# Kernel tuning notes

Hardware: AMD Instinct MI355X
Metric: run time of the kernel (lower is better)

Reference implementation:

```python
import jax, jax.numpy as jnp
import numpy as np

N, D_IN, D_EMB, K = 16384, 1024, 256, 1024
ALPHA, EPS = 0.01, 1e-5


def setup_inputs() -> dict:
    key = jax.random.key(0)
    ks = jax.random.split(key, 6)
    inp = jax.random.normal(ks[0], (N, D_IN), dtype=jnp.float32)
    W_send = jax.random.normal(ks[1], (D_IN, D_EMB), dtype=jnp.float32) / np.sqrt(D_IN)
    b_send = jnp.zeros((D_EMB,), dtype=jnp.float32)
    W_recv = jax.random.normal(ks[2], (D_EMB, D_IN), dtype=jnp.float32) / np.sqrt(D_EMB)
    b_recv = jnp.zeros((D_IN,), dtype=jnp.float32)
    codebook = jax.random.normal(ks[3], (K, D_EMB), dtype=jnp.float32)
    ema_vecs = codebook.copy()
    ema_size = jnp.zeros((K,), dtype=jnp.float32)
    return {"input": inp, "W_send": W_send, "b_send": b_send,
            "W_recv": W_recv, "b_recv": b_recv, "codebook": codebook,
            "ema_vecs": ema_vecs, "ema_size": ema_size}


def reference(input, W_send, b_send, W_recv, b_recv, codebook, ema_vecs, ema_size):
    sg = jax.lax.stop_gradient
    # send projection -> latent z  [N, D_EMB]
    z = input @ W_send + b_send
    # nearest-neighbor lookup: argmin_k ||e_k||^2 - 2 <z, e_k>
    sqr = jnp.sum(codebook * codebook, axis=1)          # [K]
    cov = jnp.einsum('nj,kj->nk', z, codebook)          # [N, K]
    codes = jnp.argmin(sqr - 2.0 * cov, axis=-1)        # [N] int
    # fetch embeddings (gather)
    vectors = codebook[codes]                            # [N, D_EMB]
    # mse losses, reduction='sum'
    embedding = jnp.sum((vectors - sg(z)) ** 2)
    commitment = jnp.sum((z - sg(vectors)) ** 2)
    # straight-through output
    emb_out = z + sg(vectors - z)
    # EMA accumulate (one-hot scatter == segment_sum)
    upd_vecs = jax.ops.segment_sum(z, codes, num_segments=K)              # [K, D_EMB]
    upd_size = jax.ops.segment_sum(jnp.ones((z.shape[0],), z.dtype), codes, num_segments=K)
    ema_vecs_new = ema_vecs + ALPHA * (upd_vecs - ema_vecs)
    ema_size_new = ema_size + ALPHA * (upd_size - ema_size)
    # EMA update (Laplace-smoothed centroid)
    n = jnp.sum(ema_size_new)
    coef = n / (n + K * EPS)
    size = coef * (ema_size_new + EPS)
    weight_new = ema_vecs_new / size[:, None]
    # empirical entropy of the codes in bits
    prob = jnp.bincount(codes, length=K).astype(jnp.float32) / codes.size
    ent = -jnp.sum(jnp.where(prob > 0, prob * jnp.log(prob), 0.0)) / jnp.log(2.0)
    # recv projection
    x = emb_out @ W_recv + b_recv
    return (x, codes, embedding, commitment, ent, ema_vecs_new, ema_size_new, weight_new)
```

## Files before the change

### kernel.cpp

```cpp
#include <hip/hip_runtime.h>
#include <math.h>

#define NROWS 16384
#define DIN   1024
#define DEMB  256
#define KC    1024
#define ALPHA 0.01f
#define EPSV  1e-5f
#define INV2048 4.8828125e-4f
#define CHUNK 32
#define COV_CHUNKS 8

typedef _Float16 f16;
typedef __attribute__((ext_vector_type(4)))  _Float16 f16x4;
typedef __attribute__((ext_vector_type(8)))  _Float16 f16x8;
typedef __attribute__((ext_vector_type(16))) float    f32x16;
typedef unsigned long long u64;

#define OFF_Z       0
#define OFF_R       4194304
#define OFF_SQR     5242880
#define OFF_ZH      5243904
#define OFF_ZL      7341056
#define OFF_WTH     9438208
#define OFF_WTL     9569280
#define OFF_CBH     9700352
#define OFF_CBL     9831424
#define OFF_KEYS    9962496
#define OFF_CODES   9995264
#define OFF_LIST    10011648
#define OFF_OFFS    10028032
#define OFF_UPD     10029056
#define OFF_HIST    10291200
#define OFF_CURSOR  10292224
#define OFF_LOSS    10293248
#define ZERO_LEN    264208
#define OFF_COUNTSF 10293264
#define OFF_SIZE    10294288

#define OUT_X      0
#define OUT_CODES  16777216
#define OUT_EMB    16793600
#define OUT_COMMIT 16793601
#define OUT_ENT    16793602
#define OUT_EMAV   16793603
#define OUT_EMAS   17055747
#define OUT_W      17056771

__device__ __forceinline__ void split_f32(float x, f16& h, f16& l) {
    h = (f16)x;
    l = (f16)((x - (float)h) * 2048.0f);
}

__global__ __launch_bounds__(64) void sqr_kernel(const float* __restrict__ cb,
                                                 float* __restrict__ sqr) {
    int k = blockIdx.x;
    int lane = threadIdx.x;
    float4 v = ((const float4*)cb)[k * 64 + lane];
    float s = v.x * v.x + v.y * v.y + v.z * v.z + v.w * v.w;
    for (int off = 32; off > 0; off >>= 1) s += __shfl_down(s, off, 64);
    if (lane == 0) sqr[k] = s;
}

__global__ __launch_bounds__(256) void split_wt_kernel(const float* __restrict__ W,
                                                       f16* __restrict__ wth,
                                                       f16* __restrict__ wtl) {
    int n = blockIdx.x;
    int t = threadIdx.x;
    f16x4 h4, l4;
#pragma unroll
    for (int j = 0; j < 4; ++j) {
        int k = t * 4 + j;
        float x = W[(size_t)k * DEMB + n];
        f16 h, l; split_f32(x, h, l);
        h4[j] = h; l4[j] = l;
    }
    *(f16x4*)&wth[(size_t)n * DIN + t * 4] = h4;
    *(f16x4*)&wtl[(size_t)n * DIN + t * 4] = l4;
}

__global__ __launch_bounds__(256) void split_cb_kernel(const float* __restrict__ cb,
                                                       f16* __restrict__ cbh,
                                                       f16* __restrict__ cbl) {
    int idx = (blockIdx.x * 256 + threadIdx.x) * 4;
    float4 v = *(const float4*)&cb[idx];
    f16x4 h4, l4;
    f16 h, l;
    split_f32(v.x, h, l); h4[0] = h; l4[0] = l;
    split_f32(v.y, h, l); h4[1] = h; l4[1] = l;
    split_f32(v.z, h, l); h4[2] = h; l4[2] = l;
    split_f32(v.w, h, l); h4[3] = h; l4[3] = l;
    *(f16x4*)&cbh[idx] = h4;
    *(f16x4*)&cbl[idx] = l4;
}

__global__ __launch_bounds__(512) void gemm1_mfma(const float* __restrict__ in,
                                                  const f16* __restrict__ wth,
                                                  const f16* __restrict__ wtl,
                                                  const float* __restrict__ bsend,
                                                  float* __restrict__ z,
                                                  f16* __restrict__ zh,
                                                  f16* __restrict__ zl) {
    __shared__ f16 sm[2 * 2 * 2 * 128 * 64];
    const int tid = threadIdx.x;
    const int wave = tid >> 6, lane = tid & 63;
    const int half = lane >> 5, l31 = lane & 31;
    const int wrow = wave >> 2, wcol = wave & 3;
    const int rowBase = blockIdx.y * 128;
    const int colBase = blockIdx.x * 128;

    const int sr  = tid >> 2;
    const int skq = tid & 3;
    const int sr7 = sr & 7;

    f32x16 accm[2] = {};
    f32x16 accx[2] = {};

    auto stageB = [&](int buf, int ks) {
#pragma unroll
        for (int i = 0; i < 4; ++i) {
            const int q  = wave * 4 + i;
            const int hl = q >> 4;
            const int c  = (q & 15) * 8 + (lane >> 3);
            const int p  = lane & 7;
            const int s  = p ^ (c & 7);
            const f16* src = (hl ? wtl : wth)
                           + (size_t)(colBase + c) * DIN + ks + s * 8;
            f16* dst = sm + buf * 32768 + 16384 + q * 512 + lane * 8;
            __builtin_amdgcn_global_load_lds(
                (const __attribute__((address_space(1))) void*)src,
                (__attribute__((address_space(3))) void*)dst, 16, 0, 0);
        }
    };

    auto loadA = [&](int ks, float4* av) {
        const float* src = &in[(size_t)(rowBase + sr) * DIN + ks + skq * 16];
#pragma unroll
        for (int j = 0; j < 4; ++j) av[j] = ((const float4*)src)[j];
    };

    auto writeA = [&](int buf, const float4* av) {
        f16* Abase = sm + buf * 32768;
#pragma unroll
        for (int q = 0; q < 2; ++q) {
            f16x8 h8, l8;
#pragma unroll
            for (int j = 0; j < 2; ++j) {
                float4 v = av[q * 2 + j];
                f16 h, l;
                split_f32(v.x, h, l); h8[j * 4 + 0] = h; l8[j * 4 + 0] = l;
                split_f32(v.y, h, l); h8[j * 4 + 1] = h; l8[j * 4 + 1] = l;
                split_f32(v.z, h, l); h8[j * 4 + 2] = h; l8[j * 4 + 2] = l;
                split_f32(v.w, h, l); h8[j * 4 + 3] = h; l8[j * 4 + 3] = l;
            }
            const int s = skq * 2 + q;
            const int off = sr * 64 + ((s ^ sr7) << 3);
            *(f16x8*)&Abase[off] = h8;
            *(f16x8*)&Abase[8192 + off] = l8;
        }
    };

    auto compute = [&](int buf) {
        const f16* Ah = sm + buf * 32768;
        const f16* Al = Ah + 8192;
        const f16* Bh = Ah + 16384;
        const f16* Bl = Ah + 24576;
        const int c  = wcol * 32 + l31;
        const int c7 = c & 7;
#pragma unroll
        for (int t4 = 0; t4 < 4; ++t4) {
            const int s = t4 * 2 + half;
            f16x8 a_h[2], a_l[2];
#pragma unroll
            for (int rt = 0; rt < 2; ++rt) {
                const int r = wrow * 64 + rt * 32 + l31;
                const int off = r * 64 + ((s ^ (r & 7)) << 3);
                a_h[rt] = *(const f16x8*)&Ah[off];
                a_l[rt] = *(const f16x8*)&Al[off];
            }
            const int boff = c * 64 + ((s ^ c7) << 3);
            f16x8 b_h = *(const f16x8*)&Bh[boff];
            f16x8 b_l = *(const f16x8*)&Bl[boff];
#pragma unroll
            for (int rt = 0; rt < 2; ++rt) {
                accm[rt] = __builtin_amdgcn_mfma_f32_32x32x16_f16(a_h[rt], b_h, accm[rt], 0, 0, 0);
                accx[rt] = __builtin_amdgcn_mfma_f32_32x32x16_f16(a_h[rt], b_l, accx[rt], 0, 0, 0);
                accx[rt] = __builtin_amdgcn_mfma_f32_32x32x16_f16(a_l[rt], b_h, accx[rt], 0, 0, 0);
            }
        }
    };

    stageB(0, 0);
    {
        float4 av[4];
        loadA(0, av);
        writeA(0, av);
    }
    __syncthreads();

    int cur = 0;
    for (int step = 0; step < 16; ++step) {
        float4 av[4];
        const bool pf = (step + 1) < 16;
        if (pf) {
            stageB(cur ^ 1, (step + 1) * 64);
            loadA((step + 1) * 64, av);
        }
        compute(cur);
        if (pf) writeA(cur ^ 1, av);
        __syncthreads();
        cur ^= 1;
    }

#pragma unroll
    for (int rt = 0; rt < 2; ++rt) {
        const int col = colBase + wcol * 32 + l31;
        const float bb = bsend[col];
#pragma unroll
        for (int reg = 0; reg < 16; ++reg) {
            const int row = rowBase + wrow * 64 + rt * 32 + (reg & 3) + 8 * (reg >> 2) + 4 * half;
            const float zv = accm[rt][reg] + INV2048 * accx[rt][reg] + bb;
            const size_t o = (size_t)row * DEMB + col;
            z[o] = zv;
            f16 h = (f16)zv;
            zh[o] = h;
            zl[o] = (f16)((zv - (float)h) * 2048.0f);
        }
    }
}

__device__ __forceinline__ void cov_stage(const f16* __restrict__ cbh,
                                          const f16* __restrict__ cbl,
                                          f16* sC, int buf, int codeBase,
                                          int wave, int lane) {
#pragma unroll
    for (int i = 0; i < 8; ++i) {
        const int seg = wave * 8 + i;
        const int hl  = seg >> 4;
        const int rp  = seg & 15;
        const int r   = rp * 2 + (lane >> 5);
        const f16* src = (hl ? cbl : cbh)
                       + (size_t)(codeBase + r) * DEMB
                       + (((lane & 31) ^ r) << 3);
        f16* dst = sC + (((buf << 1) + hl) * 32 + rp * 2) * DEMB;
        __builtin_amdgcn_global_load_lds(
            (const __attribute__((address_space(1))) void*)src,
            (__attribute__((address_space(3))) void*)dst,
            16, 0, 0);
    }
}

__global__ __launch_bounds__(256, 2) void cov_mfma_kernel(const f16* __restrict__ zh,
                                                          const f16* __restrict__ zl,
                                                          const f16* __restrict__ cbh,
                                                          const f16* __restrict__ cbl,
                                                          const float* __restrict__ sqr,
                                                          u64* __restrict__ keys) {
    __shared__ f16 sC[2 * 2 * 32 * DEMB];
    const int tid = threadIdx.x;
    const int wave = tid >> 6, lane = tid & 63;
    const int half = lane >> 5, l31 = lane & 31;
    const int rowBase = blockIdx.y * 128 + wave * 32;
    const int myRow = rowBase + l31;
    const int cb0 = blockIdx.x * (COV_CHUNKS * 32);

    cov_stage(cbh, cbl, sC, 0, cb0, wave, lane);

    f16x8 a_h[16], a_l[16];
#pragma unroll
    for (int t = 0; t < 16; ++t) {
        size_t o = (size_t)myRow * DEMB + t * 16 + half * 8;
        a_h[t] = *(const f16x8*)&zh[o];
        a_l[t] = *(const f16x8*)&zl[o];
    }

    float runv[16];
    int   runc[16];
#pragma unroll
    for (int r = 0; r < 16; ++r) { runv[r] = 3.4e38f; runc[r] = 0; }

    for (int cc = 0; cc < COV_CHUNKS; ++cc) {
        __syncthreads();
        if (cc + 1 < COV_CHUNKS)
            cov_stage(cbh, cbl, sC, (cc + 1) & 1, cb0 + (cc + 1) * 32, wave, lane);

        const f16* Ch = sC + ((cc & 1) * 2 + 0) * 32 * DEMB;
        const f16* Cl = sC + ((cc & 1) * 2 + 1) * 32 * DEMB;

        f32x16 accm = {};
        f32x16 accx = {};
#pragma unroll
        for (int t = 0; t < 16; ++t) {
            const int seg = t * 2 + half;
            const int p = ((seg ^ l31) << 3);
            f16x8 b_h = *(const f16x8*)&Ch[l31 * DEMB + p];
            f16x8 b_l = *(const f16x8*)&Cl[l31 * DEMB + p];
            accm = __builtin_amdgcn_mfma_f32_32x32x16_f16(a_h[t], b_h, accm, 0, 0, 0);
            accx = __builtin_amdgcn_mfma_f32_32x32x16_f16(a_h[t], b_l, accx, 0, 0, 0);
            accx = __builtin_amdgcn_mfma_f32_32x32x16_f16(a_l[t], b_h, accx, 0, 0, 0);
        }

        const int code = cb0 + cc * 32 + l31;
        const float sqv = sqr[code];
#pragma unroll
        for (int r = 0; r < 16; ++r) {
            float s = sqv - 2.0f * (accm[r] + INV2048 * accx[r]);
            if (s < runv[r]) { runv[r] = s; runc[r] = code; }
        }
    }

#pragma unroll
    for (int r = 0; r < 16; ++r) {
        float v = runv[r]; int ci = runc[r];
        for (int off = 16; off > 0; off >>= 1) {
            float ov = __shfl_down(v, off, 32);
            int   oc = __shfl_down(ci, off, 32);
            if (ov < v || (ov == v && oc < ci)) { v = ov; ci = oc; }
        }
        if (l31 == 0) {
            int row = rowBase + (r & 3) + 8 * (r >> 2) + 4 * half;
            unsigned ub = __float_as_uint(v);
            ub = (ub & 0x80000000u) ? ~ub : (ub | 0x80000000u);
            u64 key = ((u64)ub << 32) | (unsigned)ci;
            atomicMin(&keys[row], key);
        }
    }
}

__global__ __launch_bounds__(256) void decode_kernel(const u64* __restrict__ keys,
                                                     int* __restrict__ codes,
                                                     float* __restrict__ out_codes,
                                                     int* __restrict__ hist) {
    int r = blockIdx.x * 256 + threadIdx.x;
    int c = (int)(keys[r] & 0xFFFFFFFFull);
    codes[r] = c;
    out_codes[r] = (float)c;
    atomicAdd(&hist[c], 1);
}

__global__ __launch_bounds__(1024) void prefix_kernel(const int* __restrict__ hist,
                                                      int* __restrict__ offs,
                                                      float* __restrict__ countsf) {
    __shared__ int s[1024];
    int t = threadIdx.x;
    int v = hist[t];
    s[t] = v;
    countsf[t] = (float)v;
    __syncthreads();
    for (int d = 1; d < 1024; d <<= 1) {
        int x = (t >= d) ? s[t - d] : 0;
        __syncthreads();
        s[t] += x;
        __syncthreads();
    }
    offs[t] = s[t] - v;
}

__global__ __launch_bounds__(256) void fill_kernel(const int* __restrict__ codes,
                                                   const int* __restrict__ offs,
                                                   int* __restrict__ cursor,
                                                   int* __restrict__ list) {
    int r = blockIdx.x * 256 + threadIdx.x;
    int c = codes[r];
    int pos = offs[c] + atomicAdd(&cursor[c], 1);
    list[pos] = r;
}

__global__ __launch_bounds__(256) void upd_loss_kernel(const float* __restrict__ z,
                                                       const float* __restrict__ cb,
                                                       const int* __restrict__ list,
                                                       const int* __restrict__ codes,
                                                       float* __restrict__ upd,
                                                       float* __restrict__ loss) {
    __shared__ int srow[CHUNK];
    __shared__ int scode[CHUNK];
    const int tid = threadIdx.x;
    const int base = blockIdx.x * CHUNK;
    if (tid < CHUNK) {
        int r = list[base + tid];
        srow[tid] = r;
        scode[tid] = codes[r];
    }
    __syncthreads();

    int cur = scode[0];
    float cbv = cb[(size_t)cur * DEMB + tid];
    float acc = 0.f, lacc = 0.f;
    float zv = z[(size_t)srow[0] * DEMB + tid];
#pragma unroll 4
    for (int i = 0; i < CHUNK; ++i) {
        float znext = (i + 1 < CHUNK) ? z[(size_t)srow[i + 1] * DEMB + tid] : 0.f;
        int c = scode[i];
        if (c != cur) {
            atomicAdd(&upd[(size_t)cur * DEMB + tid], acc);
            acc = 0.f;
            cur = c;
            cbv = cb[(size_t)cur * DEMB + tid];
        }
        acc += zv;
        float d = zv - cbv;
        lacc += d * d;
        zv = znext;
    }
    atomicAdd(&upd[(size_t)cur * DEMB + tid], acc);

    __shared__ float red[256];
    red[tid] = lacc;
    __syncthreads();
    for (int s = 128; s > 0; s >>= 1) {
        if (tid < s) red[tid] += red[tid + s];
        __syncthreads();
    }
    if (tid == 0) atomicAdd(loss, red[0]);
}

__global__ __launch_bounds__(256) void gemm64_kernel(const float* __restrict__ A,
                                                     const float* __restrict__ B,
                                                     float* __restrict__ C,
                                                     int M, int Kd, int Nc) {
    __shared__ float As[16][68];
    __shared__ float Bs[16][64];
    const int tid = threadIdx.x;
    const int tx = tid & 15, ty = tid >> 4;
    const int rowBase = blockIdx.y * 64;
    const int colBase = blockIdx.x * 64;

    float acc[4][4];
#pragma unroll
    for (int i = 0; i < 4; ++i)
#pragma unroll
        for (int j = 0; j < 4; ++j) acc[i][j] = 0.f;

    const int a_row = tid >> 2;
    const int a_c4  = (tid & 3) * 4;
    const int b_r   = tid >> 4;
    const int b_c4  = (tid & 15) * 4;

    for (int kk = 0; kk < Kd; kk += 16) {
        float4 av = *(const float4*)&A[(size_t)(rowBase + a_row) * Kd + kk + a_c4];
        float4 bv = *(const float4*)&B[(size_t)(kk + b_r) * Nc + colBase + b_c4];
        __syncthreads();
        As[a_c4 + 0][a_row] = av.x;  As[a_c4 + 1][a_row] = av.y;
        As[a_c4 + 2][a_row] = av.z;  As[a_c4 + 3][a_row] = av.w;
        *(float4*)&Bs[b_r][b_c4] = bv;
        __syncthreads();
#pragma unroll
        for (int d = 0; d < 16; ++d) {
            float4 a01 = *(const float4*)&As[d][ty * 4];
            float4 b01 = *(const float4*)&Bs[d][tx * 4];
            float a[4] = {a01.x, a01.y, a01.z, a01.w};
            float b[4] = {b01.x, b01.y, b01.z, b01.w};
#pragma unroll
            for (int i = 0; i < 4; ++i)
#pragma unroll
                for (int j = 0; j < 4; ++j) acc[i][j] += a[i] * b[j];
        }
    }

#pragma unroll
    for (int i = 0; i < 4; ++i) {
        int r = rowBase + ty * 4 + i;
        *(float4*)&C[(size_t)r * Nc + colBase + tx * 4] =
            make_float4(acc[i][0], acc[i][1], acc[i][2], acc[i][3]);
    }
}

__global__ __launch_bounds__(256) void recv_kernel(const float* __restrict__ R,
                                                   const float* __restrict__ brecv,
                                                   const int* __restrict__ codes,
                                                   float* __restrict__ out) {
    const int n = blockIdx.x;
    const int t = threadIdx.x;
    const int code = codes[n];
    float4 r = ((const float4*)(R + (size_t)code * DIN))[t];
    float4 b = ((const float4*)brecv)[t];
    ((float4*)(out + (size_t)n * DIN))[t] =
        make_float4(r.x + b.x, r.y + b.y, r.z + b.z, r.w + b.w);
}

__global__ __launch_bounds__(1024) void ema_small_kernel(const float* __restrict__ ema_size,
                                                         const float* __restrict__ counts,
                                                         const float* __restrict__ loss,
                                                         float* __restrict__ size_ws,
                                                         float* __restrict__ out) {
    __shared__ float rn[1024];
    __shared__ float re[1024];
    const int k = threadIdx.x;
    float c  = counts[k];
    float es = ema_size[k];
    float esn = es + ALPHA * (c - es);
    out[OUT_EMAS + k] = esn;
    float p = c * (1.0f / (float)NROWS);
    rn[k] = esn;
    re[k] = (p > 0.f) ? p * logf(p) : 0.f;
    __syncthreads();
    for (int s = 512; s > 0; s >>= 1) {
        if (k < s) { rn[k] += rn[k + s]; re[k] += re[k + s]; }
        __syncthreads();
    }
    float n = rn[0];
    float coef = n / (n + (float)KC * EPSV);
    size_ws[k] = coef * (esn + EPSV);
    if (k == 0) {
        out[OUT_ENT] = -re[0] / logf(2.0f);
        float l = loss[0];
        out[OUT_EMB] = l;
        out[OUT_COMMIT] = l;
    }
}

__global__ __launch_bounds__(256) void emav_kernel(const float* __restrict__ ema_vecs,
                                                   const float* __restrict__ upd,
                                                   const float* __restrict__ size_ws,
                                                   float* __restrict__ out) {
    int idx = blockIdx.x * 256 + threadIdx.x;
    float ev = ema_vecs[idx], uv = upd[idx];
    float evn = ev + ALPHA * (uv - ev);
    out[OUT_EMAV + idx] = evn;
    out[OUT_W + idx] = evn / size_ws[idx >> 8];
}

extern "C" void kernel_launch(void* const* d_in, const int* in_sizes, int n_in,
                              void* d_out, int out_size, void* d_ws, size_t ws_size,
                              hipStream_t stream) {
    const float* input    = (const float*)d_in[0];
    const float* W_send   = (const float*)d_in[1];
    const float* b_send   = (const float*)d_in[2];
    const float* W_recv   = (const float*)d_in[3];
    const float* b_recv   = (const float*)d_in[4];
    const float* codebook = (const float*)d_in[5];
    const float* ema_vecs = (const float*)d_in[6];
    const float* ema_size = (const float*)d_in[7];
    float* out = (float*)d_out;
    float* ws  = (float*)d_ws;
    int*   wsi = (int*)d_ws;

    f16* wth = (f16*)(ws + OFF_WTH);
    f16* wtl = (f16*)(ws + OFF_WTL);
    f16* cbh = (f16*)(ws + OFF_CBH);
    f16* cbl = (f16*)(ws + OFF_CBL);
    f16* zh  = (f16*)(ws + OFF_ZH);
    f16* zl  = (f16*)(ws + OFF_ZL);
    u64* keys = (u64*)(ws + OFF_KEYS);

    (void)hipMemsetAsync(ws + OFF_UPD, 0, (size_t)ZERO_LEN * sizeof(float), stream);
    (void)hipMemsetAsync(ws + OFF_KEYS, 0xFF, (size_t)NROWS * sizeof(u64), stream);

    sqr_kernel<<<KC, 64, 0, stream>>>(codebook, ws + OFF_SQR);
    split_wt_kernel<<<DEMB, 256, 0, stream>>>(W_send, wth, wtl);
    split_cb_kernel<<<256, 256, 0, stream>>>(codebook, cbh, cbl);

    gemm64_kernel<<<dim3(DIN / 64, KC / 64), 256, 0, stream>>>(
        codebook, W_recv, ws + OFF_R, KC, DEMB, DIN);

    gemm1_mfma<<<dim3(DEMB / 128, NROWS / 128), 512, 0, stream>>>(
        input, wth, wtl, b_send, ws + OFF_Z, zh, zl);

    cov_mfma_kernel<<<dim3(KC / (COV_CHUNKS * 32), NROWS / 128), 256, 0, stream>>>(
        zh, zl, cbh, cbl, ws + OFF_SQR, keys);

    decode_kernel<<<NROWS / 256, 256, 0, stream>>>(
        keys, wsi + OFF_CODES, out + OUT_CODES, wsi + OFF_HIST);

    prefix_kernel<<<1, 1024, 0, stream>>>(
        wsi + OFF_HIST, wsi + OFF_OFFS, ws + OFF_COUNTSF);

    fill_kernel<<<NROWS / 256, 256, 0, stream>>>(
        wsi + OFF_CODES, wsi + OFF_OFFS, wsi + OFF_CURSOR, wsi + OFF_LIST);

    upd_loss_kernel<<<NROWS / CHUNK, 256, 0, stream>>>(
        ws + OFF_Z, codebook, wsi + OFF_LIST, wsi + OFF_CODES,
        ws + OFF_UPD, ws + OFF_LOSS);

    recv_kernel<<<NROWS, 256, 0, stream>>>(
        ws + OFF_R, b_recv, wsi + OFF_CODES, out + OUT_X);

    ema_small_kernel<<<1, 1024, 0, stream>>>(
        ema_size, ws + OFF_COUNTSF, ws + OFF_LOSS, ws + OFF_SIZE, out);

    emav_kernel<<<KC, 256, 0, stream>>>(
        ema_vecs, ws + OFF_UPD, ws + OFF_SIZE, out);
}
```

Before: 277.3 us.

## Fuse prep kernels and memsets, use MFMA for codebook·W_recv, remap block order

Replaces two memsets and three small prep kernels with a single prep_kernel that also splits W_recv into fp16 hi/lo parts and initializes the workspace buffers. The scalar fp32 gemm64 for codebook@W_recv becomes a split-fp16 MFMA kernel (gemm2_mfma) that stages W_recv hi/lo in the zh region before gemm1 overwrites it. gemm1 and cov kernels switch to 1D grids with a swizzled block-to-tile mapping meant to improve L2 reuse. The aim is to cut launch overhead and the cost of the small GEMM, at the price of split-fp16 precision in R.

```diff
diff --git a/kernel.cpp b/kernel.cpp
--- a/kernel.cpp
+++ b/kernel.cpp
@@ -34,7 +34,6 @@
 #define OFF_HIST    10291200
 #define OFF_CURSOR  10292224
 #define OFF_LOSS    10293248
-#define ZERO_LEN    264208
 #define OFF_COUNTSF 10293264
 #define OFF_SIZE    10294288
 
@@ -52,46 +51,78 @@
     l = (f16)((x - (float)h) * 2048.0f);
 }
 
-__global__ __launch_bounds__(64) void sqr_kernel(const float* __restrict__ cb,
-                                                 float* __restrict__ sqr) {
-    int k = blockIdx.x;
-    int lane = threadIdx.x;
-    float4 v = ((const float4*)cb)[k * 64 + lane];
-    float s = v.x * v.x + v.y * v.y + v.z * v.z + v.w * v.w;
-    for (int off = 32; off > 0; off >>= 1) s += __shfl_down(s, off, 64);
-    if (lane == 0) sqr[k] = s;
-}
-
-__global__ __launch_bounds__(256) void split_wt_kernel(const float* __restrict__ W,
-                                                       f16* __restrict__ wth,
-                                                       f16* __restrict__ wtl) {
-    int n = blockIdx.x;
-    int t = threadIdx.x;
-    f16x4 h4, l4;
-#pragma unroll
-    for (int j = 0; j < 4; ++j) {
-        int k = t * 4 + j;
-        float x = W[(size_t)k * DEMB + n];
-        f16 h, l; split_f32(x, h, l);
-        h4[j] = h; l4[j] = l;
-    }
-    *(f16x4*)&wth[(size_t)n * DIN + t * 4] = h4;
-    *(f16x4*)&wtl[(size_t)n * DIN + t * 4] = l4;
-}
-
-__global__ __launch_bounds__(256) void split_cb_kernel(const float* __restrict__ cb,
-                                                       f16* __restrict__ cbh,
-                                                       f16* __restrict__ cbl) {
-    int idx = (blockIdx.x * 256 + threadIdx.x) * 4;
-    float4 v = *(const float4*)&cb[idx];
-    f16x4 h4, l4;
-    f16 h, l;
-    split_f32(v.x, h, l); h4[0] = h; l4[0] = l;
-    split_f32(v.y, h, l); h4[1] = h; l4[1] = l;
-    split_f32(v.z, h, l); h4[2] = h; l4[2] = l;
-    split_f32(v.w, h, l); h4[3] = h; l4[3] = l;
-    *(f16x4*)&cbh[idx] = h4;
-    *(f16x4*)&cbl[idx] = l4;
+__global__ __launch_bounds__(256) void prep_kernel(const float* __restrict__ W_send,
+                                                   const float* __restrict__ W_recv,
+                                                   const float* __restrict__ cb,
+                                                   float* __restrict__ ws) {
+    const int b = blockIdx.x;
+    const int t = threadIdx.x;
+    int* wsi = (int*)ws;
+
+    if (b < 256) {
+        f16* wth = (f16*)(ws + OFF_WTH);
+        f16* wtl = (f16*)(ws + OFF_WTL);
+        const int n = b;
+        f16x4 h4, l4;
+#pragma unroll
+        for (int j = 0; j < 4; ++j) {
+            int k = t * 4 + j;
+            float x = W_send[(size_t)k * DEMB + n];
+            f16 h, l; split_f32(x, h, l);
+            h4[j] = h; l4[j] = l;
+        }
+        *(f16x4*)&wth[(size_t)n * DIN + t * 4] = h4;
+        *(f16x4*)&wtl[(size_t)n * DIN + t * 4] = l4;
+    } else if (b < 512) {
+        f16* cbh = (f16*)(ws + OFF_CBH);
+        f16* cbl = (f16*)(ws + OFF_CBL);
+        int idx = ((b - 256) * 256 + t) * 4;
+        float4 v = *(const float4*)&cb[idx];
+        f16x4 h4, l4;
+        f16 h, l;
+        split_f32(v.x, h, l); h4[0] = h; l4[0] = l;
+        split_f32(v.y, h, l); h4[1] = h; l4[1] = l;
+        split_f32(v.z, h, l); h4[2] = h; l4[2] = l;
+        split_f32(v.w, h, l); h4[3] = h; l4[3] = l;
+        *(f16x4*)&cbh[idx] = h4;
+        *(f16x4*)&cbl[idx] = l4;
+    } else if (b < 768) {
+        f16* wrh = (f16*)(ws + OFF_ZH);
+        f16* wrl = (f16*)(ws + OFF_ZH + 131072);
+        const int n = (b - 512) * 4 + (t >> 6);
+        const int lane = t & 63;
+        f16x4 h4, l4;
+#pragma unroll
+        for (int j = 0; j < 4; ++j) {
+            int k = lane * 4 + j;
+            float x = W_recv[(size_t)k * DIN + n];
+            f16 h, l; split_f32(x, h, l);
+            h4[j] = h; l4[j] = l;
+        }
+        *(f16x4*)&wrh[(size_t)n * DEMB + lane * 4] = h4;
+        *(f16x4*)&wrl[(size_t)n * DEMB + lane * 4] = l4;
+    } else if (b < 1024) {
+        float* sqr = ws + OFF_SQR;
+        const int k = (b - 768) * 4 + (t >> 6);
+        const int lane = t & 63;
+        float4 v = ((const float4*)cb)[k * 64 + lane];
+        float s = v.x * v.x + v.y * v.y + v.z * v.z + v.w * v.w;
+        for (int off = 32; off > 0; off >>= 1) s += __shfl_down(s, off, 64);
+        if (lane == 0) sqr[k] = s;
+    } else if (b < 1280) {
+        float4 zed = make_float4(0.f, 0.f, 0.f, 0.f);
+        *(float4*)&ws[OFF_UPD + (size_t)(b - 1024) * 1024 + t * 4] = zed;
+    } else if (b == 1280) {
+#pragma unroll
+        for (int j = 0; j < 4; ++j) {
+            wsi[OFF_HIST + t * 4 + j] = 0;
+            wsi[OFF_CURSOR + t * 4 + j] = 0;
+        }
+        if (t < 16) ws[OFF_LOSS + t] = 0.f;
+    } else {
+        u64* keys = (u64*)(ws + OFF_KEYS);
+        keys[(b - 1281) * 256 + t] = ~0ull;
+    }
 }
 
 __global__ __launch_bounds__(512) void gemm1_mfma(const float* __restrict__ in,
@@ -106,8 +137,13 @@
     const int wave = tid >> 6, lane = tid & 63;
     const int half = lane >> 5, l31 = lane & 31;
     const int wrow = wave >> 2, wcol = wave & 3;
-    const int rowBase = blockIdx.y * 128;
-    const int colBase = blockIdx.x * 128;
+
+    const int L = blockIdx.x;
+    const int v = L >> 3;
+    const int bx = v & 1;
+    const int by = (L & 7) + 8 * (v >> 1);
+    const int rowBase = by * 128;
+    const int colBase = bx * 128;
 
     const int sr  = tid >> 2;
     const int skq = tid & 3;
@@ -146,12 +182,12 @@
             f16x8 h8, l8;
 #pragma unroll
             for (int j = 0; j < 2; ++j) {
-                float4 v = av[q * 2 + j];
+                float4 v4 = av[q * 2 + j];
                 f16 h, l;
-                split_f32(v.x, h, l); h8[j * 4 + 0] = h; l8[j * 4 + 0] = l;
-                split_f32(v.y, h, l); h8[j * 4 + 1] = h; l8[j * 4 + 1] = l;
-                split_f32(v.z, h, l); h8[j * 4 + 2] = h; l8[j * 4 + 2] = l;
-                split_f32(v.w, h, l); h8[j * 4 + 3] = h; l8[j * 4 + 3] = l;
+                split_f32(v4.x, h, l); h8[j * 4 + 0] = h; l8[j * 4 + 0] = l;
+                split_f32(v4.y, h, l); h8[j * 4 + 1] = h; l8[j * 4 + 1] = l;
+                split_f32(v4.z, h, l); h8[j * 4 + 2] = h; l8[j * 4 + 2] = l;
+                split_f32(v4.w, h, l); h8[j * 4 + 3] = h; l8[j * 4 + 3] = l;
             }
             const int s = skq * 2 + q;
             const int off = sr * 64 + ((s ^ sr7) << 3);
@@ -226,6 +262,67 @@
             zh[o] = h;
             zl[o] = (f16)((zv - (float)h) * 2048.0f);
         }
+    }
+}
+
+__global__ __launch_bounds__(256, 2) void gemm2_mfma(const f16* __restrict__ cbh,
+                                                     const f16* __restrict__ cbl,
+                                                     const f16* __restrict__ wrh,
+                                                     const f16* __restrict__ wrl,
+                                                     float* __restrict__ R) {
+    __shared__ f16 sm[16384];
+    const int tid = threadIdx.x;
+    const int wave = tid >> 6, lane = tid & 63;
+    const int half = lane >> 5, l31 = lane & 31;
+    const int wr = wave >> 1, wc = wave & 1;
+    const int rowBase = blockIdx.y * 64;
+    const int colBase = blockIdx.x * 64;
+
+    f32x16 accm = {}, accx = {};
+
+    for (int step = 0; step < 4; ++step) {
+        const int ks = step * 64;
+        __syncthreads();
+#pragma unroll
+        for (int i = 0; i < 8; ++i) {
+            const int q   = wave * 8 + i;
+            const int arr = q >> 3;
+            const int grp = q & 7;
+            const int r   = grp * 8 + (lane >> 3);
+            const int p   = lane & 7;
+            const int s   = p ^ (r & 7);
+            const f16* basep = (arr == 0) ? cbh : (arr == 1) ? cbl
+                             : (arr == 2) ? wrh : wrl;
+            const int rowg = ((arr >= 2) ? colBase : rowBase) + r;
+            const f16* src = basep + (size_t)rowg * DEMB + ks + s * 8;
+            f16* dst = sm + arr * 4096 + grp * 512;
+            __builtin_amdgcn_global_load_lds(
+                (const __attribute__((address_space(1))) void*)src,
+                (__attribute__((address_space(3))) void*)dst, 16, 0, 0);
+        }
+        __syncthreads();
+#pragma unroll
+        for (int t = 0; t < 4; ++t) {
+            const int sgi = t * 2 + half;
+            const int ar = wr * 32 + l31;
+            const int bc = wc * 32 + l31;
+            const int aoff = ar * 64 + ((sgi ^ (ar & 7)) << 3);
+            const int boff = bc * 64 + ((sgi ^ (bc & 7)) << 3);
+            f16x8 a_h = *(const f16x8*)&sm[aoff];
+            f16x8 a_l = *(const f16x8*)&sm[4096 + aoff];
+            f16x8 b_h = *(const f16x8*)&sm[8192 + boff];
+            f16x8 b_l = *(const f16x8*)&sm[12288 + boff];
+            accm = __builtin_amdgcn_mfma_f32_32x32x16_f16(a_h, b_h, accm, 0, 0, 0);
+            accx = __builtin_amdgcn_mfma_f32_32x32x16_f16(a_h, b_l, accx, 0, 0, 0);
+            accx = __builtin_amdgcn_mfma_f32_32x32x16_f16(a_l, b_h, accx, 0, 0, 0);
+        }
+    }
+
+    const int col = colBase + wc * 32 + l31;
+#pragma unroll
+    for (int reg = 0; reg < 16; ++reg) {
+        const int row = rowBase + wr * 32 + (reg & 3) + 8 * (reg >> 2) + 4 * half;
+        R[(size_t)row * DIN + col] = accm[reg] + INV2048 * accx[reg];
     }
 }
 
@@ -260,9 +357,15 @@
     const int tid = threadIdx.x;
     const int wave = tid >> 6, lane = tid & 63;
     const int half = lane >> 5, l31 = lane & 31;
-    const int rowBase = blockIdx.y * 128 + wave * 32;
+
+    const int L = blockIdx.x;
+    const int v = L >> 3;
+    const int bx = v & 3;
+    const int by = (L & 7) + 8 * (v >> 2);
+
+    const int rowBase = by * 128 + wave * 32;
     const int myRow = rowBase + l31;
-    const int cb0 = blockIdx.x * (COV_CHUNKS * 32);
+    const int cb0 = bx * (COV_CHUNKS * 32);
 
     cov_stage(cbh, cbl, sC, 0, cb0, wave, lane);
 
@@ -311,15 +414,15 @@
 
 #pragma unroll
     for (int r = 0; r < 16; ++r) {
-        float v = runv[r]; int ci = runc[r];
+        float v2 = runv[r]; int ci = runc[r];
         for (int off = 16; off > 0; off >>= 1) {
-            float ov = __shfl_down(v, off, 32);
+            float ov = __shfl_down(v2, off, 32);
             int   oc = __shfl_down(ci, off, 32);
-            if (ov < v || (ov == v && oc < ci)) { v = ov; ci = oc; }
+            if (ov < v2 || (ov == v2 && oc < ci)) { v2 = ov; ci = oc; }
         }
         if (l31 == 0) {
             int row = rowBase + (r & 3) + 8 * (r >> 2) + 4 * half;
-            unsigned ub = __float_as_uint(v);
+            unsigned ub = __float_as_uint(v2);
             ub = (ub & 0x80000000u) ? ~ub : (ub | 0x80000000u);
             u64 key = ((u64)ub << 32) | (unsigned)ci;
             atomicMin(&keys[row], key);
@@ -412,57 +515,6 @@
         __syncthreads();
     }
     if (tid == 0) atomicAdd(loss, red[0]);
-}
-
-__global__ __launch_bounds__(256) void gemm64_kernel(const float* __restrict__ A,
-                                                     const float* __restrict__ B,
-                                                     float* __restrict__ C,
-                                                     int M, int Kd, int Nc) {
-    __shared__ float As[16][68];
-    __shared__ float Bs[16][64];
-    const int tid = threadIdx.x;
-    const int tx = tid & 15, ty = tid >> 4;
-    const int rowBase = blockIdx.y * 64;
-    const int colBase = blockIdx.x * 64;
-
-    float acc[4][4];
-#pragma unroll
-    for (int i = 0; i < 4; ++i)
-#pragma unroll
-        for (int j = 0; j < 4; ++j) acc[i][j] = 0.f;
-
-    const int a_row = tid >> 2;
-    const int a_c4  = (tid & 3) * 4;
-    const int b_r   = tid >> 4;
-    const int b_c4  = (tid & 15) * 4;
-
-    for (int kk = 0; kk < Kd; kk += 16) {
-        float4 av = *(const float4*)&A[(size_t)(rowBase + a_row) * Kd + kk + a_c4];
-        float4 bv = *(const float4*)&B[(size_t)(kk + b_r) * Nc + colBase + b_c4];
-        __syncthreads();
-        As[a_c4 + 0][a_row] = av.x;  As[a_c4 + 1][a_row] = av.y;
-        As[a_c4 + 2][a_row] = av.z;  As[a_c4 + 3][a_row] = av.w;
-        *(float4*)&Bs[b_r][b_c4] = bv;
-        __syncthreads();
-#pragma unroll
-        for (int d = 0; d < 16; ++d) {
-            float4 a01 = *(const float4*)&As[d][ty * 4];
-            float4 b01 = *(const float4*)&Bs[d][tx * 4];
-            float a[4] = {a01.x, a01.y, a01.z, a01.w};
-            float b[4] = {b01.x, b01.y, b01.z, b01.w};
-#pragma unroll
-            for (int i = 0; i < 4; ++i)
-#pragma unroll
-                for (int j = 0; j < 4; ++j) acc[i][j] += a[i] * b[j];
-        }
-    }
-
-#pragma unroll
-    for (int i = 0; i < 4; ++i) {
-        int r = rowBase + ty * 4 + i;
-        *(float4*)&C[(size_t)r * Nc + colBase + tx * 4] =
-            make_float4(acc[i][0], acc[i][1], acc[i][2], acc[i][3]);
-    }
 }
 
 __global__ __launch_bounds__(256) void recv_kernel(const float* __restrict__ R,
@@ -542,21 +594,18 @@
     f16* zh  = (f16*)(ws + OFF_ZH);
     f16* zl  = (f16*)(ws + OFF_ZL);
     u64* keys = (u64*)(ws + OFF_KEYS);
-
-    (void)hipMemsetAsync(ws + OFF_UPD, 0, (size_t)ZERO_LEN * sizeof(float), stream);
-    (void)hipMemsetAsync(ws + OFF_KEYS, 0xFF, (size_t)NROWS * sizeof(u64), stream);
-
-    sqr_kernel<<<KC, 64, 0, stream>>>(codebook, ws + OFF_SQR);
-    split_wt_kernel<<<DEMB, 256, 0, stream>>>(W_send, wth, wtl);
-    split_cb_kernel<<<256, 256, 0, stream>>>(codebook, cbh, cbl);
-
-    gemm64_kernel<<<dim3(DIN / 64, KC / 64), 256, 0, stream>>>(
-        codebook, W_recv, ws + OFF_R, KC, DEMB, DIN);
-
-    gemm1_mfma<<<dim3(DEMB / 128, NROWS / 128), 512, 0, stream>>>(
+    f16* wrh = (f16*)(ws + OFF_ZH);
+    f16* wrl = (f16*)(ws + OFF_ZH + 131072);
+
+    prep_kernel<<<1345, 256, 0, stream>>>(W_send, W_recv, codebook, ws);
+
+    gemm2_mfma<<<dim3(DIN / 64, KC / 64), 256, 0, stream>>>(
+        cbh, cbl, wrh, wrl, ws + OFF_R);
+
+    gemm1_mfma<<<(DEMB / 128) * (NROWS / 128), 512, 0, stream>>>(
         input, wth, wtl, b_send, ws + OFF_Z, zh, zl);
 
-    cov_mfma_kernel<<<dim3(KC / (COV_CHUNKS * 32), NROWS / 128), 256, 0, stream>>>(
+    cov_mfma_kernel<<<(KC / (COV_CHUNKS * 32)) * (NROWS / 128), 256, 0, stream>>>(
         zh, zl, cbh, cbl, ws + OFF_SQR, keys);
 
     decode_kernel<<<NROWS / 256, 256, 0, stream>>>(
```

New measurement: 253.0 us (median of 3 runs). -8.8%, faster.
